# Performance work log

Hardware: AMD Instinct MI355X
Metric: run time of the kernel (lower is better)

The kernel has to match this reference:

```python
import jax, jax.numpy as jnp
import numpy as np

BETA = 1.0
N = 8192


def setup_inputs() -> dict:
    key = jax.random.key(0)
    k1, k2 = jax.random.split(key)
    pred = jax.random.normal(k1, (N,), dtype=jnp.float32)
    target = jax.random.normal(k2, (N,), dtype=jnp.float32)
    return {"pred": pred, "target": target}


def reference(pred, target) -> jnp.ndarray:
    # Pairwise diffs: [N, N]
    pred_diff = pred[:, None] - pred[None, :]
    target_diff = target[:, None] - target[None, :]
    n = pred.shape[0]
    # Upper triangle (i < j), excluding diagonal; only pairs with t_i != t_j count.
    iu = jnp.arange(n)
    triu = iu[:, None] < iu[None, :]
    valid = triu & (target_diff != 0)
    # For pair (i, j) with i < j: if t_i > t_j use (p_i - p_j), else (p_j - p_i)
    # => signed diff = sign(t_i - t_j) * (p_i - p_j). Note target_diff[i, j] = t_i - t_j
    # with our [:, None]-[None, :] convention matches pred_diff[i, j] = p_i - p_j.
    s = jnp.sign(target_diff)
    # log(1 + exp(-beta * s * pred_diff)) = softplus(-beta * s * pred_diff), numerically stable.
    per_pair = jax.nn.softplus(-BETA * s * pred_diff)
    loss_sum = jnp.sum(jnp.where(valid, per_pair, 0.0))
    num_pairs = jnp.sum(valid).astype(pred.dtype)
    return jnp.where(num_pairs > 0, loss_sum / num_pairs, 0.0)
```

## Files before the change

kernel.cpp:

```cpp
#include <hip/hip_runtime.h>


#define TJ 1024
#define TI 32
#define RATIO (TJ / TI)
#define NT 256
#define LOG2E 1.44269504088896340736f
#define LN2   0.69314718055994530942f

__device__ __forceinline__ void pair_op(float ti, float pi, float tjv, float pjv,
                                        bool iok, float neg_inf,
                                        float& prod, float& sumH, unsigned int& cnt)
{
    const float td = ti - tjv;
    const float pd = pi - pjv;
    float z = (td > 0.f) ? -pd : pd;
    const bool valid = (td != 0.f) & iok;
    z = valid ? z : neg_inf;
    cnt += (unsigned int)__popcll(__ballot(valid));
    const float e = __builtin_amdgcn_exp2f(-LOG2E * __builtin_fabsf(z));
    prod = __builtin_fmaf(prod, e, prod);
    sumH += __builtin_fmaxf(z, 0.f);
}

__global__ __launch_bounds__(NT, 8) void rank_pairs_kernel(
    const float* __restrict__ pred, const float* __restrict__ target, int n,
    float* __restrict__ part_sum, unsigned int* __restrict__ part_cnt,
    unsigned int* __restrict__ done_cnt, int nblocks, float* __restrict__ out)
{
    int bx, iy, bid;
    if (gridDim.y == 1) {
        bid = (int)blockIdx.x;
        bx = (int)__builtin_sqrtf((float)bid * (2.0f / (float)RATIO));
        while ((RATIO / 2) * (bx + 1) * (bx + 2) <= bid) ++bx;
        while ((RATIO / 2) * bx * (bx + 1) > bid) --bx;
        iy = bid - (RATIO / 2) * bx * (bx + 1);
    } else {
        bx = (int)blockIdx.x; iy = (int)blockIdx.y;
        bid = iy * (int)gridDim.x + bx;
    }

    const int j_base = bx * TJ;
    const int i_base = iy * TI;
    const int j0     = j_base + (int)threadIdx.x * 4;

    __shared__ float2 s_tp[TI];

    float prod[4] = {1.f, 1.f, 1.f, 1.f};
    float sumH[4] = {0.f, 0.f, 0.f, 0.f};
    unsigned int cnt = 0u;
    const float neg_inf = -__builtin_inff();
    float sum = 0.f;

    if (gridDim.y == 1) {
        if (threadIdx.x < TI) {
            const int i = i_base + (int)threadIdx.x;
            s_tp[threadIdx.x] = make_float2(target[i], pred[i]);
        }
        __syncthreads();

        const float4 p4 = *(const float4*)(pred + j0);
        const float4 t4 = *(const float4*)(target + j0);
        const float pjv[4] = {p4.x, p4.y, p4.z, p4.w};
        const float tjv[4] = {t4.x, t4.y, t4.z, t4.w};

        if (i_base + TI <= j_base) {
            #pragma unroll 8
            for (int k = 0; k < TI; ++k) {
                const float2 tp = s_tp[k];
                #pragma unroll
                for (int jj = 0; jj < 4; ++jj)
                    pair_op(tp.x, tp.y, tjv[jj], pjv[jj], true, neg_inf,
                            prod[jj], sumH[jj], cnt);
            }
        } else {
            #pragma unroll 8
            for (int k = 0; k < TI; ++k) {
                const float2 tp = s_tp[k];
                #pragma unroll
                for (int jj = 0; jj < 4; ++jj)
                    pair_op(tp.x, tp.y, tjv[jj], pjv[jj],
                            (i_base + k) < (j0 + jj), neg_inf,
                            prod[jj], sumH[jj], cnt);
            }
        }
    } else {
        if (i_base < j_base + TJ && i_base < n) {
            for (int k = 0; k < TI; ++k) {
                const int i = i_base + k;
                if (i >= n) break;
                const float ti = target[i];
                const float pi = pred[i];
                for (int jj = 0; jj < 4; ++jj) {
                    const int  j   = j0 + jj;
                    const bool jin = (j < n);
                    const int  jc  = jin ? j : (n - 1);
                    pair_op(ti, pi, target[jc], pred[jc],
                            jin && (i < j), neg_inf, prod[jj], sumH[jj], cnt);
                }
            }
        }
    }

    const float sumW = __builtin_amdgcn_logf(prod[0] * prod[1]) +
                       __builtin_amdgcn_logf(prod[2] * prod[3]);
    sum = ((sumH[0] + sumH[1]) + (sumH[2] + sumH[3])) + LN2 * sumW;

    #pragma unroll
    for (int off = 32; off > 0; off >>= 1)
        sum += __shfl_down(sum, off, 64);

    __shared__ float        s_s[NT / 64];
    __shared__ unsigned int s_c[NT / 64];
    __shared__ bool         s_last;
    const int lane = threadIdx.x & 63;
    const int wv   = threadIdx.x >> 6;
    if (lane == 0) { s_s[wv] = sum; s_c[wv] = cnt; }
    __syncthreads();
    if (threadIdx.x == 0) {
        float bs = 0.f; unsigned int bc = 0u;
        #pragma unroll
        for (int w = 0; w < NT / 64; ++w) { bs += s_s[w]; bc += s_c[w]; }
        part_sum[bid] = bs;
        part_cnt[bid] = bc;
        __threadfence();
        const unsigned int prev = atomicAdd(done_cnt, 1u);
        s_last = (prev == (unsigned int)(nblocks - 1));
    }
    __syncthreads();

    if (s_last) {
        __threadfence();
        float fs = 0.f; unsigned int fc = 0u;
        for (int idx = (int)threadIdx.x; idx < nblocks; idx += NT) {
            fs += part_sum[idx];
            fc += part_cnt[idx];
        }
        #pragma unroll
        for (int off = 32; off > 0; off >>= 1) {
            fs += __shfl_down(fs, off, 64);
            fc += __shfl_down(fc, off, 64);
        }
        if (lane == 0) { s_s[wv] = fs; s_c[wv] = fc; }
        __syncthreads();
        if (threadIdx.x == 0) {
            float bs = 0.f; unsigned int bc = 0u;
            #pragma unroll
            for (int w = 0; w < NT / 64; ++w) { bs += s_s[w]; bc += s_c[w]; }
            out[0] = (bc > 0u) ? bs / (float)bc : 0.f;
        }
    }
}

extern "C" void kernel_launch(void* const* d_in, const int* in_sizes, int n_in,
                              void* d_out, int out_size, void* d_ws, size_t ws_size,
                              hipStream_t stream)
{
    const float* pred   = (const float*)d_in[0];
    const float* target = (const float*)d_in[1];
    float* out = (float*)d_out;
    const int n = in_sizes[0];

    dim3 grid;
    int nblocks;
    if (n >= TJ && (n % TJ == 0)) {
        const int gx = n / TJ;
        nblocks = (RATIO / 2) * gx * (gx + 1);
        grid = dim3((unsigned)nblocks, 1);
    } else {
        const int gx = (n + TJ - 1) / TJ;
        const int gy = (n + TI - 1) / TI;
        nblocks = gx * gy;
        grid = dim3((unsigned)gx, (unsigned)gy);
    }

    float*        part_sum = (float*)d_ws;
    unsigned int* part_cnt = (unsigned int*)((char*)d_ws + (size_t)nblocks * sizeof(float));
    unsigned int* done_cnt = (unsigned int*)((char*)d_ws + (size_t)2 * nblocks * sizeof(float));

    hipMemsetAsync(done_cnt, 0, sizeof(unsigned int), stream);
    rank_pairs_kernel<<<grid, NT, 0, stream>>>(pred, target, n, part_sum, part_cnt,
                                               done_cnt, nblocks, out);
}
```

Baseline: 83.86 us.

## Rewrite softplus via |z| identity and correct masked pairs with closed-form term

Uses max(z,0) = (|z|+z)/2 to accumulate |pd| and a signed sum separately instead of a per-pair max. Invalid pairs now contribute log(2) via exp(0) rather than being masked with -inf, and that excess is subtracted once at the end using the total pair count. Halves the j-tile to 512 with 2 columns per thread, which doubles the block count and shrinks the per-thread register footprint. The single large final correction term adds risk of float32 cancellation error.

```diff
diff --git a/kernel.cpp b/kernel.cpp
--- a/kernel.cpp
+++ b/kernel.cpp
@@ -1,32 +1,19 @@
 #include <hip/hip_runtime.h>
 
 
-#define TJ 1024
+#define TJ 512
 #define TI 32
 #define RATIO (TJ / TI)
 #define NT 256
+#define JPT (TJ / NT)
 #define LOG2E 1.44269504088896340736f
 #define LN2   0.69314718055994530942f
-
-__device__ __forceinline__ void pair_op(float ti, float pi, float tjv, float pjv,
-                                        bool iok, float neg_inf,
-                                        float& prod, float& sumH, unsigned int& cnt)
-{
-    const float td = ti - tjv;
-    const float pd = pi - pjv;
-    float z = (td > 0.f) ? -pd : pd;
-    const bool valid = (td != 0.f) & iok;
-    z = valid ? z : neg_inf;
-    cnt += (unsigned int)__popcll(__ballot(valid));
-    const float e = __builtin_amdgcn_exp2f(-LOG2E * __builtin_fabsf(z));
-    prod = __builtin_fmaf(prod, e, prod);
-    sumH += __builtin_fmaxf(z, 0.f);
-}
 
 __global__ __launch_bounds__(NT, 8) void rank_pairs_kernel(
     const float* __restrict__ pred, const float* __restrict__ target, int n,
     float* __restrict__ part_sum, unsigned int* __restrict__ part_cnt,
-    unsigned int* __restrict__ done_cnt, int nblocks, float* __restrict__ out)
+    unsigned int* __restrict__ done_cnt, int nblocks, float p_total,
+    float* __restrict__ out)
 {
     int bx, iy, bid;
     if (gridDim.y == 1) {
@@ -42,14 +29,13 @@
 
     const int j_base = bx * TJ;
     const int i_base = iy * TI;
-    const int j0     = j_base + (int)threadIdx.x * 4;
+    const int j0     = j_base + (int)threadIdx.x * JPT;
 
     __shared__ float2 s_tp[TI];
 
-    float prod[4] = {1.f, 1.f, 1.f, 1.f};
-    float sumH[4] = {0.f, 0.f, 0.f, 0.f};
+    float prod[JPT] = {1.f, 1.f};
+    float A = 0.f, B = 0.f;
     unsigned int cnt = 0u;
-    const float neg_inf = -__builtin_inff();
     float sum = 0.f;
 
     if (gridDim.y == 1) {
@@ -59,52 +45,79 @@
         }
         __syncthreads();
 
-        const float4 p4 = *(const float4*)(pred + j0);
-        const float4 t4 = *(const float4*)(target + j0);
-        const float pjv[4] = {p4.x, p4.y, p4.z, p4.w};
-        const float tjv[4] = {t4.x, t4.y, t4.z, t4.w};
+        const float2 p2 = *(const float2*)(pred + j0);
+        const float2 t2 = *(const float2*)(target + j0);
+        const float pjv[JPT] = {p2.x, p2.y};
+        const float tjv[JPT] = {t2.x, t2.y};
 
         if (i_base + TI <= j_base) {
             #pragma unroll 8
             for (int k = 0; k < TI; ++k) {
                 const float2 tp = s_tp[k];
                 #pragma unroll
-                for (int jj = 0; jj < 4; ++jj)
-                    pair_op(tp.x, tp.y, tjv[jj], pjv[jj], true, neg_inf,
-                            prod[jj], sumH[jj], cnt);
+                for (int jj = 0; jj < JPT; ++jj) {
+                    const bool  gt    = tp.x > tjv[jj];
+                    const bool  valid = tp.x != tjv[jj];
+                    const float pd    = tp.y - pjv[jj];
+                    const float pdm   = valid ? pd : 0.f;
+                    cnt += (unsigned int)__popcll(__ballot(valid));
+                    A += __builtin_fabsf(pdm);
+                    B += gt ? pdm : -pdm;
+                    const float e = __builtin_amdgcn_exp2f(-LOG2E * __builtin_fabsf(pdm));
+                    prod[jj] = __builtin_fmaf(prod[jj], e, prod[jj]);
+                }
             }
         } else {
             #pragma unroll 8
             for (int k = 0; k < TI; ++k) {
                 const float2 tp = s_tp[k];
+                const int i = i_base + k;
                 #pragma unroll
-                for (int jj = 0; jj < 4; ++jj)
-                    pair_op(tp.x, tp.y, tjv[jj], pjv[jj],
-                            (i_base + k) < (j0 + jj), neg_inf,
-                            prod[jj], sumH[jj], cnt);
+                for (int jj = 0; jj < JPT; ++jj) {
+                    const bool  iok   = i < (j0 + jj);
+                    const bool  gt    = tp.x > tjv[jj];
+                    const bool  valid = (tp.x != tjv[jj]) & iok;
+                    const float pd    = tp.y - pjv[jj];
+                    const float pdm   = valid ? pd : 0.f;
+                    cnt += (unsigned int)__popcll(__ballot(valid));
+                    A += __builtin_fabsf(pdm);
+                    B += gt ? pdm : -pdm;
+                    const float e = __builtin_amdgcn_exp2f(-LOG2E * __builtin_fabsf(pdm));
+                    prod[jj] = __builtin_fmaf(prod[jj], e, prod[jj]);
+                }
             }
         }
+        const float W = __builtin_amdgcn_logf(prod[0] * prod[1]);
+        sum = 0.5f * (A - B) + LN2 * W;
     } else {
+        const float neg_inf = -__builtin_inff();
+        float sumH = 0.f;
         if (i_base < j_base + TJ && i_base < n) {
             for (int k = 0; k < TI; ++k) {
                 const int i = i_base + k;
                 if (i >= n) break;
                 const float ti = target[i];
                 const float pi = pred[i];
-                for (int jj = 0; jj < 4; ++jj) {
+                for (int jj = 0; jj < JPT; ++jj) {
                     const int  j   = j0 + jj;
                     const bool jin = (j < n);
                     const int  jc  = jin ? j : (n - 1);
-                    pair_op(ti, pi, target[jc], pred[jc],
-                            jin && (i < j), neg_inf, prod[jj], sumH[jj], cnt);
+                    const float tj = target[jc], pj = pred[jc];
+                    const float td = ti - tj;
+                    const float pd = pi - pj;
+                    float z = (td > 0.f) ? -pd : pd;
+                    const bool valid = (td != 0.f) && jin && (i < j);
+                    z = valid ? z : neg_inf;
+                    cnt += (unsigned int)__popcll(__ballot(valid));
+                    const float e = __builtin_amdgcn_exp2f(-LOG2E * __builtin_fabsf(z));
+                    prod[jj] = __builtin_fmaf(prod[jj], e, prod[jj]);
+                    sumH += __builtin_fmaxf(z, 0.f);
                 }
             }
         }
-    }
-
-    const float sumW = __builtin_amdgcn_logf(prod[0] * prod[1]) +
-                       __builtin_amdgcn_logf(prod[2] * prod[3]);
-    sum = ((sumH[0] + sumH[1]) + (sumH[2] + sumH[3])) + LN2 * sumW;
+        const float W = __builtin_amdgcn_logf(prod[0] * prod[1]);
+        sum = sumH + LN2 * W;
+    }
 
     #pragma unroll
     for (int off = 32; off > 0; off >>= 1)
@@ -147,6 +160,7 @@
             float bs = 0.f; unsigned int bc = 0u;
             #pragma unroll
             for (int w = 0; w < NT / 64; ++w) { bs += s_s[w]; bc += s_c[w]; }
+            if (p_total > 0.f) bs -= LN2 * (p_total - (float)bc);
             out[0] = (bc > 0u) ? bs / (float)bc : 0.f;
         }
     }
@@ -163,15 +177,18 @@
 
     dim3 grid;
     int nblocks;
+    float p_total;
     if (n >= TJ && (n % TJ == 0)) {
         const int gx = n / TJ;
         nblocks = (RATIO / 2) * gx * (gx + 1);
         grid = dim3((unsigned)nblocks, 1);
+        p_total = (float)((long long)nblocks * TJ * TI);
     } else {
         const int gx = (n + TJ - 1) / TJ;
         const int gy = (n + TI - 1) / TI;
         nblocks = gx * gy;
         grid = dim3((unsigned)gx, (unsigned)gy);
+        p_total = 0.f;
     }
 
     float*        part_sum = (float*)d_ws;
@@ -180,5 +197,5 @@
 
     hipMemsetAsync(done_cnt, 0, sizeof(unsigned int), stream);
     rank_pairs_kernel<<<grid, NT, 0, stream>>>(pred, target, n, part_sum, part_cnt,
-                                               done_cnt, nblocks, out);
+                                               done_cnt, nblocks, p_total, out);
 }
```

Measured after the change: 103.8 us. 1.24x slower.
